# Kernel tuning notes

Hardware: AMD Instinct MI355X
Metric: run time of the kernel (lower is better)

The kernel has to match this reference:

```python
import jax, jax.numpy as jnp
import numpy as np

N, E = 50000, 800000
H, F, R = 256, 128, 32  # hidden_channels, graph_convolution_filters, radial_dim
EPS = 1e-5


def layernorm(x, g, b):
    mu = jnp.mean(x, axis=-1, keepdims=True)
    var = jnp.mean(jnp.square(x - mu), axis=-1, keepdims=True)
    return (x - mu) * jax.lax.rsqrt(var + EPS) * g + b


def setup_inputs() -> dict:
    key = jax.random.key(0)
    ks = jax.random.split(key, 12)
    s = 0.02
    return {
        "x": jax.random.normal(ks[0], (N, H), jnp.float32),
        "rbf": jax.random.normal(ks[1], (E, R), jnp.float32),
        "edge_index": jax.random.randint(ks[2], (2, E), 0, N, jnp.int32),
        # node_to_message: Linear(H -> F)
        "ntm_w": jax.random.normal(ks[3], (F, H), jnp.float32) * s,
        "ntm_b": jnp.zeros((F,), jnp.float32),
        # radial_to_message: Linear(R -> F)
        "rtm_w": jax.random.normal(ks[4], (F, R), jnp.float32) * s,
        "rtm_b": jnp.zeros((F,), jnp.float32),
        # outer Normalization (layer)
        "norm_g": jnp.ones((F,), jnp.float32),
        "norm_b": jnp.zeros((F,), jnp.float32),
        # MPConv linear1: Linear(3F -> F)
        "l1_w": jax.random.normal(ks[5], (F, 3 * F), jnp.float32) * s,
        "l1_b": jnp.zeros((F,), jnp.float32),
        # MPConv LayerNorm(F)
        "ln_g": jnp.ones((F,), jnp.float32),
        "ln_b": jnp.zeros((F,), jnp.float32),
        # MPConv linear2: Linear(F -> F)
        "l2_w": jax.random.normal(ks[6], (F, F), jnp.float32) * s,
        "l2_b": jnp.zeros((F,), jnp.float32),
        # message_to_node: Linear(F -> H, bias=False)
        "mtn_w": jax.random.normal(ks[7], (H, F), jnp.float32) * s,
    }


def reference(x, rbf, edge_index, ntm_w, ntm_b, rtm_w, rtm_b, norm_g, norm_b,
              l1_w, l1_b, ln_g, ln_b, l2_w, l2_b, mtn_w):
    # edge_attr = radial_to_message(rbf)
    edge_attr = rbf @ rtm_w.T + rtm_b                      # [E, F]
    # x = Normalization('layer')(node_to_message(x))
    xf = layernorm(x @ ntm_w.T + ntm_b, norm_g, norm_b)    # [N, F]
    i, j = edge_index[0], edge_index[1]
    # MPConv: cat(x[i], x[j], edge_attr) -> linear1 -> LN -> GELU -> linear2
    cat = jnp.concatenate((xf[i], xf[j], edge_attr), axis=-1)  # [E, 3F]
    h = layernorm(cat @ l1_w.T + l1_b, ln_g, ln_b)
    m = jax.nn.gelu(h, approximate=False) @ l2_w.T + l2_b      # [E, F]
    agg = jax.ops.segment_sum(m, j, num_segments=x.shape[0])   # [N, F]
    # message_to_node (no bias)
    return agg @ mtn_w.T                                       # [N, H]
```

## Files before the change

### kernel.cpp

```cpp
#include <hip/hip_runtime.h>
#include <math.h>

#define HD 256
#define FD 128
#define RD 32
#define K1DIM 288
#define EB 64
#define LNEPS 1e-5f

typedef const float* fp;
typedef unsigned short ushort_t;
typedef __attribute__((ext_vector_type(8))) short s16x8;
typedef __attribute__((ext_vector_type(4))) float f32x4;

__device__ __forceinline__ ushort_t f2bf(float f) {
    union { float f; unsigned int u; } v; v.f = f;
    unsigned int r = v.u + 0x7fffu + ((v.u >> 16) & 1u);
    return (ushort_t)(r >> 16);
}

__global__ __launch_bounds__(128) void prep_weights(
    fp __restrict__ l1_w, fp __restrict__ l1_b,
    fp __restrict__ rtm_w, fp __restrict__ rtm_b, fp __restrict__ l2_w,
    fp __restrict__ ntm_w, fp __restrict__ mtn_w,
    ushort_t* __restrict__ W1p, ushort_t* __restrict__ W2p,
    float* __restrict__ bias1p,
    ushort_t* __restrict__ W0p, ushort_t* __restrict__ Wm)
{
    const int n = blockIdx.x;
    const int t = threadIdx.x;
    __shared__ float c[FD];
    c[t] = l1_w[n * 3 * FD + 2 * FD + t];
    W1p[n * K1DIM + t]      = f2bf(l1_w[n * 3 * FD + t]);
    W1p[n * K1DIM + FD + t] = f2bf(l1_w[n * 3 * FD + FD + t]);
    W2p[n * FD + t]         = f2bf(l2_w[n * FD + t]);
    W0p[n * HD + t]         = f2bf(ntm_w[n * HD + t]);
    W0p[n * HD + FD + t]    = f2bf(ntm_w[n * HD + FD + t]);
    Wm[n * FD + t]              = f2bf(mtn_w[n * FD + t]);
    Wm[(n + FD) * FD + t]       = f2bf(mtn_w[(n + FD) * FD + t]);
    __syncthreads();
    if (t < RD) {
        float a = 0.f;
        for (int f = 0; f < FD; ++f) a += c[f] * rtm_w[f * RD + t];
        W1p[n * K1DIM + 2 * FD + t] = f2bf(a);
    }
    if (t == 64) {
        float a = l1_b[n];
        for (int f = 0; f < FD; ++f) a += c[f] * rtm_b[f];
        bias1p[n] = a;
    }
}

__global__ __launch_bounds__(256, 2) void node_xform_mfma(
    fp __restrict__ x, const ushort_t* __restrict__ W0p,
    fp __restrict__ ntm_b, fp __restrict__ norm_g, fp __restrict__ norm_b,
    ushort_t* __restrict__ xfb, int N, int ntiles)
{
    __shared__ __attribute__((aligned(16))) ushort_t A[EB][HD + 8];
    __shared__ __attribute__((aligned(16))) float ssum[EB][4];
    __shared__ __attribute__((aligned(16))) float ssq[EB][4];
    __shared__ float smu[EB], sinv[EB];

    const int t    = threadIdx.x;
    const int w    = t >> 6;
    const int lane = t & 63;
    const int q    = lane >> 4;
    const int lq   = lane & 15;
    const int n0   = w * 32;

    s16x8 b0[8][2];
    float biasv[2], gv[2], bv[2];
    #pragma unroll
    for (int s = 0; s < 2; ++s) {
        const int n = n0 + s * 16 + lq;
        #pragma unroll
        for (int kt = 0; kt < 8; ++kt)
            b0[kt][s] = *(const s16x8*)(W0p + n * HD + kt * 32 + q * 8);
        biasv[s] = ntm_b[n];
        gv[s]    = norm_g[n];
        bv[s]    = norm_b[n];
    }

    for (int tile = blockIdx.x; tile < ntiles; tile += gridDim.x) {
        {
            const int row = t >> 2, cc = (t & 3) * 64;
            const long n = (long)tile * EB + row;
            if (n < N) {
                const float4* src = (const float4*)(x + n * HD + cc);
                #pragma unroll
                for (int c = 0; c < 8; ++c) {
                    float4 u0 = src[2 * c], u1 = src[2 * c + 1];
                    ushort_t tmp[8] = { f2bf(u0.x), f2bf(u0.y), f2bf(u0.z), f2bf(u0.w),
                                        f2bf(u1.x), f2bf(u1.y), f2bf(u1.z), f2bf(u1.w) };
                    *(s16x8*)&A[row][cc + c * 8] = *(s16x8*)tmp;
                }
            } else {
                s16x8 z = (s16x8)0;
                #pragma unroll
                for (int c = 0; c < 8; ++c)
                    *(s16x8*)&A[row][cc + c * 8] = z;
            }
        }
        __syncthreads();

        f32x4 c1[4][2];
        #pragma unroll
        for (int mt = 0; mt < 4; ++mt)
            #pragma unroll
            for (int s = 0; s < 2; ++s) {
                c1[mt][s][0] = biasv[s]; c1[mt][s][1] = biasv[s];
                c1[mt][s][2] = biasv[s]; c1[mt][s][3] = biasv[s];
            }
        #pragma unroll
        for (int kt = 0; kt < 8; ++kt) {
            s16x8 a[4];
            #pragma unroll
            for (int mt = 0; mt < 4; ++mt)
                a[mt] = *(const s16x8*)&A[mt * 16 + lq][kt * 32 + q * 8];
            #pragma unroll
            for (int mt = 0; mt < 4; ++mt)
                #pragma unroll
                for (int s = 0; s < 2; ++s)
                    c1[mt][s] = __builtin_amdgcn_mfma_f32_16x16x32_bf16(
                        a[mt], b0[kt][s], c1[mt][s], 0, 0, 0);
        }

        {
            float sv[4][4], sq2[4][4];
            #pragma unroll
            for (int mt = 0; mt < 4; ++mt)
                #pragma unroll
                for (int r = 0; r < 4; ++r) {
                    float a = c1[mt][0][r], b = c1[mt][1][r];
                    sv[mt][r]  = a + b;
                    sq2[mt][r] = a * a + b * b;
                }
            #pragma unroll
            for (int m = 1; m < 16; m <<= 1)
                #pragma unroll
                for (int mt = 0; mt < 4; ++mt)
                    #pragma unroll
                    for (int r = 0; r < 4; ++r) {
                        sv[mt][r]  += __shfl_xor(sv[mt][r], m);
                        sq2[mt][r] += __shfl_xor(sq2[mt][r], m);
                    }
            if (lq == 0) {
                #pragma unroll
                for (int mt = 0; mt < 4; ++mt)
                    #pragma unroll
                    for (int r = 0; r < 4; ++r) {
                        const int row = mt * 16 + q * 4 + r;
                        ssum[row][w] = sv[mt][r];
                        ssq[row][w]  = sq2[mt][r];
                    }
            }
        }
        __syncthreads();
        if (t < EB) {
            float4 s4 = *(const float4*)ssum[t];
            float4 q4 = *(const float4*)ssq[t];
            const float tot  = s4.x + s4.y + s4.z + s4.w;
            const float totq = q4.x + q4.y + q4.z + q4.w;
            const float mu   = tot * (1.0f / FD);
            float var = totq * (1.0f / FD) - mu * mu;
            smu[t]  = mu;
            sinv[t] = rsqrtf(var + LNEPS);
        }
        __syncthreads();

        #pragma unroll
        for (int mt = 0; mt < 4; ++mt)
            #pragma unroll
            for (int r = 0; r < 4; ++r) {
                const int row = mt * 16 + q * 4 + r;
                const long n = (long)tile * EB + row;
                if (n < N) {
                    const float mu = smu[row], inv = sinv[row];
                    #pragma unroll
                    for (int s = 0; s < 2; ++s)
                        xfb[n * FD + n0 + s * 16 + lq] =
                            f2bf((c1[mt][s][r] - mu) * inv * gv[s] + bv[s]);
                }
            }
        __syncthreads();
    }
}

__global__ __launch_bounds__(256, 4) void edge_mlp_mfma(
    fp __restrict__ rbf, const int* __restrict__ ei, int E, int ntiles,
    const ushort_t* __restrict__ W1p, const ushort_t* __restrict__ W2p,
    const float* __restrict__ bias1p,
    fp __restrict__ ln_g, fp __restrict__ ln_b, fp __restrict__ l2_b,
    const ushort_t* __restrict__ xfb, float* __restrict__ agg)
{
    __shared__ __attribute__((aligned(16))) ushort_t A1[EB][K1DIM + 8];
    __shared__ __attribute__((aligned(16))) float ssum[EB][4];
    __shared__ __attribute__((aligned(16))) float ssq[EB][4];
    __shared__ float smu[EB], sinv[EB];
    __shared__ int jrow[EB];
    ushort_t (*A2)[FD + 8] = (ushort_t (*)[FD + 8])(&A1[0][0]);

    const int t    = threadIdx.x;
    const int w    = t >> 6;
    const int lane = t & 63;
    const int q    = lane >> 4;
    const int lq   = lane & 15;
    const int n0   = w * 32;

    const ushort_t* w1r[2];
    #pragma unroll
    for (int s = 0; s < 2; ++s)
        w1r[s] = W1p + (size_t)(n0 + s * 16 + lq) * K1DIM + q * 8;

    s16x8 b2[4][2];
    #pragma unroll
    for (int s = 0; s < 2; ++s) {
        const int n = n0 + s * 16 + lq;
        #pragma unroll
        for (int kt = 0; kt < 4; ++kt)
            b2[kt][s] = *(const s16x8*)(W2p + n * FD + kt * 32 + q * 8);
    }
    float g_ln[2], bb_ln[2], bias1v[2], bias2v[2];
    #pragma unroll
    for (int s = 0; s < 2; ++s) {
        const int n = n0 + s * 16 + lq;
        g_ln[s]   = ln_g[n];
        bb_ln[s]  = ln_b[n];
        bias1v[s] = bias1p[n];
        bias2v[s] = l2_b[n];
    }

    for (int tile = blockIdx.x; tile < ntiles; tile += gridDim.x) {
        {
            const int el = t >> 2, p = t & 3;
            const long e = (long)tile * EB + el;
            if (e < E) {
                const int inode = ei[e];
                const int jnode = ei[(long)E + e];
                if (p == 0) jrow[el] = jnode;
                const s16x8* si = (const s16x8*)(xfb + (long)inode * FD + p * 32);
                const s16x8* sj = (const s16x8*)(xfb + (long)jnode * FD + p * 32);
                s16x8* di = (s16x8*)&A1[el][p * 32];
                s16x8* dj = (s16x8*)&A1[el][FD + p * 32];
                #pragma unroll
                for (int c = 0; c < 4; ++c) { di[c] = si[c]; dj[c] = sj[c]; }
                const float* rs = rbf + e * RD + p * 8;
                ushort_t tmp[8];
                #pragma unroll
                for (int c = 0; c < 8; ++c) tmp[c] = f2bf(rs[c]);
                *(s16x8*)&A1[el][2 * FD + p * 8] = *(s16x8*)tmp;
            } else {
                if (p == 0) jrow[el] = -1;
                s16x8 z = (s16x8)0;
                #pragma unroll
                for (int c = 0; c < 4; ++c) {
                    ((s16x8*)&A1[el][p * 32])[c] = z;
                    ((s16x8*)&A1[el][FD + p * 32])[c] = z;
                }
                *(s16x8*)&A1[el][2 * FD + p * 8] = z;
            }
        }
        __syncthreads();

        f32x4 c1[4][2];
        #pragma unroll
        for (int mt = 0; mt < 4; ++mt)
            #pragma unroll
            for (int s = 0; s < 2; ++s) {
                c1[mt][s][0] = bias1v[s]; c1[mt][s][1] = bias1v[s];
                c1[mt][s][2] = bias1v[s]; c1[mt][s][3] = bias1v[s];
            }
        #pragma unroll
        for (int kt = 0; kt < 9; ++kt) {
            s16x8 b1s[2];
            #pragma unroll
            for (int s = 0; s < 2; ++s)
                b1s[s] = *(const s16x8*)(w1r[s] + kt * 32);
            s16x8 a[4];
            #pragma unroll
            for (int mt = 0; mt < 4; ++mt)
                a[mt] = *(const s16x8*)&A1[mt * 16 + lq][kt * 32 + q * 8];
            #pragma unroll
            for (int mt = 0; mt < 4; ++mt)
                #pragma unroll
                for (int s = 0; s < 2; ++s)
                    c1[mt][s] = __builtin_amdgcn_mfma_f32_16x16x32_bf16(
                        a[mt], b1s[s], c1[mt][s], 0, 0, 0);
        }

        {
            float sv[4][4], sq2[4][4];
            #pragma unroll
            for (int mt = 0; mt < 4; ++mt)
                #pragma unroll
                for (int r = 0; r < 4; ++r) {
                    float a = c1[mt][0][r], b = c1[mt][1][r];
                    sv[mt][r]  = a + b;
                    sq2[mt][r] = a * a + b * b;
                }
            #pragma unroll
            for (int m = 1; m < 16; m <<= 1)
                #pragma unroll
                for (int mt = 0; mt < 4; ++mt)
                    #pragma unroll
                    for (int r = 0; r < 4; ++r) {
                        sv[mt][r]  += __shfl_xor(sv[mt][r], m);
                        sq2[mt][r] += __shfl_xor(sq2[mt][r], m);
                    }
            if (lq == 0) {
                #pragma unroll
                for (int mt = 0; mt < 4; ++mt)
                    #pragma unroll
                    for (int r = 0; r < 4; ++r) {
                        const int row = mt * 16 + q * 4 + r;
                        ssum[row][w] = sv[mt][r];
                        ssq[row][w]  = sq2[mt][r];
                    }
            }
        }
        __syncthreads();
        if (t < EB) {
            float4 s4 = *(const float4*)ssum[t];
            float4 q4 = *(const float4*)ssq[t];
            const float tot  = s4.x + s4.y + s4.z + s4.w;
            const float totq = q4.x + q4.y + q4.z + q4.w;
            const float mu   = tot * (1.0f / FD);
            float var = totq * (1.0f / FD) - mu * mu;
            smu[t]  = mu;
            sinv[t] = rsqrtf(var + LNEPS);
        }
        __syncthreads();

        #pragma unroll
        for (int mt = 0; mt < 4; ++mt)
            #pragma unroll
            for (int r = 0; r < 4; ++r) {
                const int row = mt * 16 + q * 4 + r;
                const float mu = smu[row], inv = sinv[row];
                #pragma unroll
                for (int s = 0; s < 2; ++s) {
                    float hn = (c1[mt][s][r] - mu) * inv * g_ln[s] + bb_ln[s];
                    float ge = 0.5f * hn * (1.0f + erff(hn * 0.70710678118654752f));
                    A2[row][n0 + s * 16 + lq] = f2bf(ge);
                }
            }
        __syncthreads();

        f32x4 c2[4][2];
        #pragma unroll
        for (int mt = 0; mt < 4; ++mt)
            #pragma unroll
            for (int s = 0; s < 2; ++s) {
                c2[mt][s][0] = bias2v[s]; c2[mt][s][1] = bias2v[s];
                c2[mt][s][2] = bias2v[s]; c2[mt][s][3] = bias2v[s];
            }
        #pragma unroll
        for (int kt = 0; kt < 4; ++kt) {
            s16x8 a[4];
            #pragma unroll
            for (int mt = 0; mt < 4; ++mt)
                a[mt] = *(const s16x8*)&A2[mt * 16 + lq][kt * 32 + q * 8];
            #pragma unroll
            for (int mt = 0; mt < 4; ++mt)
                #pragma unroll
                for (int s = 0; s < 2; ++s)
                    c2[mt][s] = __builtin_amdgcn_mfma_f32_16x16x32_bf16(
                        a[mt], b2[kt][s], c2[mt][s], 0, 0, 0);
        }

        #pragma unroll
        for (int mt = 0; mt < 4; ++mt)
            #pragma unroll
            for (int r = 0; r < 4; ++r) {
                const int row = mt * 16 + q * 4 + r;
                const int jj = jrow[row];
                if (jj >= 0) {
                    #pragma unroll
                    for (int s = 0; s < 2; ++s)
                        atomicAdd(&agg[(long)jj * FD + n0 + s * 16 + lq],
                                  c2[mt][s][r]);
                }
            }
        __syncthreads();
    }
}

__global__ __launch_bounds__(256, 2) void node_out_mfma(
    const float* __restrict__ agg, const ushort_t* __restrict__ Wm,
    float* __restrict__ out, int N, int ntiles)
{
    __shared__ __attribute__((aligned(16))) ushort_t A[EB][FD + 8];

    const int t    = threadIdx.x;
    const int w    = t >> 6;
    const int lane = t & 63;
    const int q    = lane >> 4;
    const int lq   = lane & 15;
    const int n0   = w * 64;

    s16x8 bm[4][4];
    #pragma unroll
    for (int s = 0; s < 4; ++s) {
        const int h = n0 + s * 16 + lq;
        #pragma unroll
        for (int kt = 0; kt < 4; ++kt)
            bm[kt][s] = *(const s16x8*)(Wm + h * FD + kt * 32 + q * 8);
    }

    for (int tile = blockIdx.x; tile < ntiles; tile += gridDim.x) {
        {
            const int row = t >> 2, cc = (t & 3) * 32;
            const long n = (long)tile * EB + row;
            if (n < N) {
                const float4* src = (const float4*)(agg + n * FD + cc);
                #pragma unroll
                for (int c = 0; c < 4; ++c) {
                    float4 u0 = src[2 * c], u1 = src[2 * c + 1];
                    ushort_t tmp[8] = { f2bf(u0.x), f2bf(u0.y), f2bf(u0.z), f2bf(u0.w),
                                        f2bf(u1.x), f2bf(u1.y), f2bf(u1.z), f2bf(u1.w) };
                    *(s16x8*)&A[row][cc + c * 8] = *(s16x8*)tmp;
                }
            } else {
                s16x8 z = (s16x8)0;
                #pragma unroll
                for (int c = 0; c < 4; ++c)
                    *(s16x8*)&A[row][cc + c * 8] = z;
            }
        }
        __syncthreads();

        f32x4 cacc[4][4];
        #pragma unroll
        for (int mt = 0; mt < 4; ++mt)
            #pragma unroll
            for (int s = 0; s < 4; ++s)
                cacc[mt][s] = (f32x4)0.0f;
        #pragma unroll
        for (int kt = 0; kt < 4; ++kt) {
            s16x8 a[4];
            #pragma unroll
            for (int mt = 0; mt < 4; ++mt)
                a[mt] = *(const s16x8*)&A[mt * 16 + lq][kt * 32 + q * 8];
            #pragma unroll
            for (int mt = 0; mt < 4; ++mt)
                #pragma unroll
                for (int s = 0; s < 4; ++s)
                    cacc[mt][s] = __builtin_amdgcn_mfma_f32_16x16x32_bf16(
                        a[mt], bm[kt][s], cacc[mt][s], 0, 0, 0);
        }

        #pragma unroll
        for (int mt = 0; mt < 4; ++mt)
            #pragma unroll
            for (int r = 0; r < 4; ++r) {
                const long n = (long)tile * EB + mt * 16 + q * 4 + r;
                if (n < N) {
                    #pragma unroll
                    for (int s = 0; s < 4; ++s)
                        out[n * HD + n0 + s * 16 + lq] = cacc[mt][s][r];
                }
            }
        __syncthreads();
    }
}

extern "C" void kernel_launch(void* const* d_in, const int* in_sizes, int n_in,
                              void* d_out, int out_size, void* d_ws, size_t ws_size,
                              hipStream_t stream) {
    fp x      = (fp)d_in[0];
    fp rbf    = (fp)d_in[1];
    const int* ei = (const int*)d_in[2];
    fp ntm_w  = (fp)d_in[3];
    fp ntm_b  = (fp)d_in[4];
    fp rtm_w  = (fp)d_in[5];
    fp rtm_b  = (fp)d_in[6];
    fp norm_g = (fp)d_in[7];
    fp norm_b = (fp)d_in[8];
    fp l1_w   = (fp)d_in[9];
    fp l1_b   = (fp)d_in[10];
    fp ln_g   = (fp)d_in[11];
    fp ln_b   = (fp)d_in[12];
    fp l2_w   = (fp)d_in[13];
    fp l2_b   = (fp)d_in[14];
    fp mtn_w  = (fp)d_in[15];

    const int N = in_sizes[0] / HD;
    const int E = in_sizes[2] / 2;

    char* wp = (char*)d_ws;
    float*    agg    = (float*)wp;              wp += (size_t)N * FD * 4;
    ushort_t* xfb    = (ushort_t*)wp;           wp += (size_t)N * FD * 2;
    ushort_t* W1p    = (ushort_t*)wp;           wp += (size_t)FD * K1DIM * 2;
    ushort_t* W2p    = (ushort_t*)wp;           wp += (size_t)FD * FD * 2;
    float*    bias1p = (float*)wp;              wp += FD * 4;
    ushort_t* W0p    = (ushort_t*)wp;           wp += (size_t)FD * HD * 2;
    ushort_t* Wm     = (ushort_t*)wp;           wp += (size_t)HD * FD * 2;

    hipMemsetAsync((void*)agg, 0, (size_t)N * FD * sizeof(float), stream);

    prep_weights<<<FD, 128, 0, stream>>>(l1_w, l1_b, rtm_w, rtm_b, l2_w,
                                         ntm_w, mtn_w, W1p, W2p, bias1p, W0p, Wm);

    const int ntilesN = (N + EB - 1) / EB;
    node_xform_mfma<<<ntilesN, 256, 0, stream>>>(x, W0p, ntm_b, norm_g, norm_b,
                                                 xfb, N, ntilesN);

    const int ntilesE = (E + EB - 1) / EB;
    const int nblk = ntilesE < 1024 ? ntilesE : 1024;
    edge_mlp_mfma<<<nblk, 256, 0, stream>>>(rbf, ei, E, ntilesE, W1p, W2p, bias1p,
                                            ln_g, ln_b, l2_b, xfb, agg);

    node_out_mfma<<<ntilesN, 256, 0, stream>>>(agg, Wm, (float*)d_out, N, ntilesN);
}
```

Baseline: 710.1 us.

## Sort edges by destination and segment-reduce messages before atomic scatter

Adds a counting sort of edges by destination node (histogram, three-pass scan, scatter into a permutation). The edge MLP then processes edges in that order and stages its outputs in shared memory. Consecutive rows with the same destination are summed before one atomicAdd, which cuts the number of global float atomics. It also prefetches the next W1 fragment one k-step ahead. The cost is six extra small kernels, an indirect gather of rbf and edge indices through the permutation, and two extra block barriers per tile.

```diff
diff --git a/kernel.cpp b/kernel.cpp
--- a/kernel.cpp
+++ b/kernel.cpp
@@ -51,6 +51,73 @@
     }
 }
 
+__global__ __launch_bounds__(256) void hist_j(
+    const int* __restrict__ ei, int E, int* __restrict__ counts)
+{
+    const int e = blockIdx.x * 256 + threadIdx.x;
+    if (e < E) atomicAdd(&counts[ei[E + e]], 1);
+}
+
+__global__ __launch_bounds__(256) void scan_blocks(
+    const int* __restrict__ counts, int N, int* __restrict__ excl,
+    int* __restrict__ tots)
+{
+    __shared__ int s[256];
+    const int tid = threadIdx.x;
+    const int idx = blockIdx.x * 256 + tid;
+    const int v = (idx < N) ? counts[idx] : 0;
+    s[tid] = v; __syncthreads();
+    #pragma unroll
+    for (int off = 1; off < 256; off <<= 1) {
+        const int a = (tid >= off) ? s[tid - off] : 0;
+        __syncthreads();
+        s[tid] += a;
+        __syncthreads();
+    }
+    if (idx < N) excl[idx] = s[tid] - v;
+    if (tid == 255) tots[blockIdx.x] = s[255];
+}
+
+__global__ __launch_bounds__(256) void scan_tops(int* __restrict__ tots, int nb)
+{
+    __shared__ int s[256];
+    const int tid = threadIdx.x;
+    const int v = (tid < nb) ? tots[tid] : 0;
+    s[tid] = v; __syncthreads();
+    #pragma unroll
+    for (int off = 1; off < 256; off <<= 1) {
+        const int a = (tid >= off) ? s[tid - off] : 0;
+        __syncthreads();
+        s[tid] += a;
+        __syncthreads();
+    }
+    if (tid < nb) tots[tid] = s[tid] - v;
+}
+
+__global__ __launch_bounds__(256) void scan_addback(
+    int* __restrict__ excl, const int* __restrict__ tots, int N,
+    int* __restrict__ cursor)
+{
+    const int idx = blockIdx.x * 256 + threadIdx.x;
+    if (idx < N) {
+        const int o = excl[idx] + tots[blockIdx.x];
+        excl[idx] = o;
+        cursor[idx] = o;
+    }
+}
+
+__global__ __launch_bounds__(256) void scatter_perm(
+    const int* __restrict__ ei, int E, int* __restrict__ cursor,
+    int* __restrict__ perm)
+{
+    const int e = blockIdx.x * 256 + threadIdx.x;
+    if (e < E) {
+        const int j = ei[E + e];
+        const int pos = atomicAdd(&cursor[j], 1);
+        perm[pos] = e;
+    }
+}
+
 __global__ __launch_bounds__(256, 2) void node_xform_mfma(
     fp __restrict__ x, const ushort_t* __restrict__ W0p,
     fp __restrict__ ntm_b, fp __restrict__ norm_g, fp __restrict__ norm_b,
@@ -187,7 +254,8 @@
 }
 
 __global__ __launch_bounds__(256, 4) void edge_mlp_mfma(
-    fp __restrict__ rbf, const int* __restrict__ ei, int E, int ntiles,
+    fp __restrict__ rbf, const int* __restrict__ ei,
+    const int* __restrict__ perm, int E, int ntiles,
     const ushort_t* __restrict__ W1p, const ushort_t* __restrict__ W2p,
     const float* __restrict__ bias1p,
     fp __restrict__ ln_g, fp __restrict__ ln_b, fp __restrict__ l2_b,
@@ -199,6 +267,7 @@
     __shared__ float smu[EB], sinv[EB];
     __shared__ int jrow[EB];
     ushort_t (*A2)[FD + 8] = (ushort_t (*)[FD + 8])(&A1[0][0]);
+    float (*c2f)[FD + 4]   = (float (*)[FD + 4])(&A1[0][0]);
 
     const int t    = threadIdx.x;
     const int w    = t >> 6;
@@ -233,8 +302,9 @@
     for (int tile = blockIdx.x; tile < ntiles; tile += gridDim.x) {
         {
             const int el = t >> 2, p = t & 3;
-            const long e = (long)tile * EB + el;
-            if (e < E) {
+            const long pos = (long)tile * EB + el;
+            if (pos < E) {
+                const int e = perm[pos];
                 const int inode = ei[e];
                 const int jnode = ei[(long)E + e];
                 if (p == 0) jrow[el] = jnode;
@@ -244,7 +314,7 @@
                 s16x8* dj = (s16x8*)&A1[el][FD + p * 32];
                 #pragma unroll
                 for (int c = 0; c < 4; ++c) { di[c] = si[c]; dj[c] = sj[c]; }
-                const float* rs = rbf + e * RD + p * 8;
+                const float* rs = rbf + (long)e * RD + p * 8;
                 ushort_t tmp[8];
                 #pragma unroll
                 for (int c = 0; c < 8; ++c) tmp[c] = f2bf(rs[c]);
@@ -270,12 +340,18 @@
                 c1[mt][s][0] = bias1v[s]; c1[mt][s][1] = bias1v[s];
                 c1[mt][s][2] = bias1v[s]; c1[mt][s][3] = bias1v[s];
             }
+        s16x8 b1n[2];
+        #pragma unroll
+        for (int s = 0; s < 2; ++s) b1n[s] = *(const s16x8*)(w1r[s]);
         #pragma unroll
         for (int kt = 0; kt < 9; ++kt) {
-            s16x8 b1s[2];
-            #pragma unroll
-            for (int s = 0; s < 2; ++s)
-                b1s[s] = *(const s16x8*)(w1r[s] + kt * 32);
+            s16x8 b1c[2];
+            b1c[0] = b1n[0]; b1c[1] = b1n[1];
+            if (kt < 8) {
+                #pragma unroll
+                for (int s = 0; s < 2; ++s)
+                    b1n[s] = *(const s16x8*)(w1r[s] + (kt + 1) * 32);
+            }
             s16x8 a[4];
             #pragma unroll
             for (int mt = 0; mt < 4; ++mt)
@@ -285,7 +361,7 @@
                 #pragma unroll
                 for (int s = 0; s < 2; ++s)
                     c1[mt][s] = __builtin_amdgcn_mfma_f32_16x16x32_bf16(
-                        a[mt], b1s[s], c1[mt][s], 0, 0, 0);
+                        a[mt], b1c[s], c1[mt][s], 0, 0, 0);
         }
 
         {
@@ -367,20 +443,36 @@
                     c2[mt][s] = __builtin_amdgcn_mfma_f32_16x16x32_bf16(
                         a[mt], b2[kt][s], c2[mt][s], 0, 0, 0);
         }
+        __syncthreads();
 
         #pragma unroll
         for (int mt = 0; mt < 4; ++mt)
             #pragma unroll
             for (int r = 0; r < 4; ++r) {
                 const int row = mt * 16 + q * 4 + r;
+                #pragma unroll
+                for (int s = 0; s < 2; ++s)
+                    c2f[row][n0 + s * 16 + lq] = c2[mt][s][r];
+            }
+        __syncthreads();
+
+        {
+            const int col = t & 127, half = t >> 7;
+            int cur = -1;
+            float acc = 0.0f;
+            #pragma unroll 4
+            for (int r = 0; r < 32; ++r) {
+                const int row = half * 32 + r;
                 const int jj = jrow[row];
-                if (jj >= 0) {
-                    #pragma unroll
-                    for (int s = 0; s < 2; ++s)
-                        atomicAdd(&agg[(long)jj * FD + n0 + s * 16 + lq],
-                                  c2[mt][s][r]);
-                }
-            }
+                if (jj != cur) {
+                    if (cur >= 0) atomicAdd(&agg[(long)cur * FD + col], acc);
+                    cur = jj;
+                    acc = 0.0f;
+                }
+                if (jj >= 0) acc += c2f[row][col];
+            }
+            if (cur >= 0) atomicAdd(&agg[(long)cur * FD + col], acc);
+        }
         __syncthreads();
     }
 }
@@ -495,11 +587,25 @@
     float*    bias1p = (float*)wp;              wp += FD * 4;
     ushort_t* W0p    = (ushort_t*)wp;           wp += (size_t)FD * HD * 2;
     ushort_t* Wm     = (ushort_t*)wp;           wp += (size_t)HD * FD * 2;
+    int*      counts = (int*)wp;                wp += (size_t)N * 4;
+    int*      offs   = (int*)wp;                wp += (size_t)N * 4;
+    int*      cursor = (int*)wp;                wp += (size_t)N * 4;
+    int*      tots   = (int*)wp;                wp += 256 * 4;
+    int*      perm   = (int*)wp;                wp += (size_t)E * 4;
 
     hipMemsetAsync((void*)agg, 0, (size_t)N * FD * sizeof(float), stream);
+    hipMemsetAsync((void*)counts, 0, (size_t)N * sizeof(int), stream);
 
     prep_weights<<<FD, 128, 0, stream>>>(l1_w, l1_b, rtm_w, rtm_b, l2_w,
                                          ntm_w, mtn_w, W1p, W2p, bias1p, W0p, Wm);
+
+    const int nbE = (E + 255) / 256;
+    const int nbN = (N + 255) / 256;
+    hist_j<<<nbE, 256, 0, stream>>>(ei, E, counts);
+    scan_blocks<<<nbN, 256, 0, stream>>>(counts, N, offs, tots);
+    scan_tops<<<1, 256, 0, stream>>>(tots, nbN);
+    scan_addback<<<nbN, 256, 0, stream>>>(offs, tots, N, cursor);
+    scatter_perm<<<nbE, 256, 0, stream>>>(ei, E, cursor, perm);
 
     const int ntilesN = (N + EB - 1) / EB;
     node_xform_mfma<<<ntilesN, 256, 0, stream>>>(x, W0p, ntm_b, norm_g, norm_b,
@@ -507,7 +613,8 @@
 
     const int ntilesE = (E + EB - 1) / EB;
     const int nblk = ntilesE < 1024 ? ntilesE : 1024;
-    edge_mlp_mfma<<<nblk, 256, 0, stream>>>(rbf, ei, E, ntilesE, W1p, W2p, bias1p,
+    edge_mlp_mfma<<<nblk, 256, 0, stream>>>(rbf, ei, perm, E, ntilesE,
+                                            W1p, W2p, bias1p,
                                             ln_g, ln_b, l2_b, xfb, agg);
 
     node_out_mfma<<<ntilesN, 256, 0, stream>>>(agg, Wm, (float*)d_out, N, ntilesN);
```

New measurement: 733.6 us. +3.3%, slower.
